# Optimization experiments

Hardware: AMD Instinct MI355X
Metric: run time of the kernel (lower is better)

## Reference

```python
import jax, jax.numpy as jnp
import numpy as np

EPS = 1e-5
GROUPS = 32


def conv2d(x, w, b):
    # x: [N,C,H,W], w: [O,I,3,3] (or 1x1), stride 1, padding 'same' for 3x3
    kh = w.shape[2]
    pad = (kh - 1) // 2
    y = jax.lax.conv_general_dilated(x, w, (1, 1), ((pad, pad), (pad, pad)),
                                     dimension_numbers=('NCHW', 'OIHW', 'NCHW'))
    return y + b[None, :, None, None]


def group_norm(x, g, b):
    N, C, H, W = x.shape
    xr = x.reshape(N, GROUPS, C // GROUPS, H, W)
    mu = xr.mean(axis=(2, 3, 4), keepdims=True)
    var = xr.var(axis=(2, 3, 4), keepdims=True)
    xr = (xr - mu) / jnp.sqrt(var + EPS)
    return xr.reshape(N, C, H, W) * g[None, :, None, None] + b[None, :, None, None]


def batch_norm(x, g, b):
    # training-mode BatchNorm2d: batch statistics over (N,H,W)
    mu = x.mean(axis=(0, 2, 3), keepdims=True)
    var = x.var(axis=(0, 2, 3), keepdims=True)
    return (x - mu) / jnp.sqrt(var + EPS) * g[None, :, None, None] + b[None, :, None, None]


def binary_activation(x):
    # STE: forward sign(x), backward through piecewise poly out3
    out_fwd = jnp.sign(x)
    m1 = (x < -1).astype(x.dtype)
    m2 = (x < 0).astype(x.dtype)
    m3 = (x < 1).astype(x.dtype)
    out1 = -1.0 * m1 + (x * x + 2.0 * x) * (1.0 - m1)
    out2 = out1 * m2 + (-x * x + 2.0 * x) * (1.0 - m2)
    out3 = out2 * m3 + 1.0 * (1.0 - m3)
    return jax.lax.stop_gradient(out_fwd - out3) + out3


def hard_binary_conv(x, w, b):
    # per-output-channel scaling * sign(w), STE through clipped weights
    scale = jax.lax.stop_gradient(jnp.mean(jnp.abs(w), axis=(1, 2, 3), keepdims=True))
    bw_ng = scale * jnp.sign(w)
    clipped = jnp.clip(w, -1.0, 1.0)
    bw = jax.lax.stop_gradient(bw_ng - clipped) + clipped
    return conv2d(x, bw, b)


def learnable_bias(x, emb, w, b):
    bias = jax.nn.silu(emb) @ w.T + b  # [B, C]
    return x + bias[:, :, None, None]


def _forward(c, x, emb,
             rb_gn1_g, rb_gn1_b, rb_conv1_w, rb_conv1_b, rb_emb_w, rb_emb_b,
             rb_gn2_g, rb_gn2_b, rb_conv2_w, rb_conv2_b,
             m1_w, m1_b, bconv_w, bconv_b, bn_g, bn_b,
             m2_w, m2_b, prelu_a, m3_w, m3_b):
    # ResBlock (skip = Identity since out_channels == channels)
    h = conv2d(jax.nn.silu(group_norm(c, rb_gn1_g, rb_gn1_b)), rb_conv1_w, rb_conv1_b)
    eo = jax.nn.silu(emb) @ rb_emb_w.T + rb_emb_b          # [B, 2*C]
    scale, shift = jnp.split(eo[:, :, None, None], 2, axis=1)
    h = group_norm(h, rb_gn2_g, rb_gn2_b) * (1.0 + scale) + shift
    h = conv2d(jax.nn.silu(h), rb_conv2_w, rb_conv2_b)
    c2 = c + h
    # concat + bias + STE binarize + binary conv + BN + channel-pool residual + PReLU
    xc = jnp.concatenate([x, c2], axis=1)                   # [B, 2C, H, W]
    out = learnable_bias(xc, emb, m1_w, m1_b)
    out = binary_activation(out)
    out = hard_binary_conv(out, bconv_w, bconv_b)
    out = batch_norm(out, bn_g, bn_b)
    N, C2, H, W = xc.shape
    out = out + xc.reshape(N, C2 // 2, 2, H, W).mean(axis=2)  # channel mean pooling
    out = learnable_bias(out, emb, m2_w, m2_b)
    out = jnp.where(out >= 0, out, prelu_a[None, :, None, None] * out)  # PReLU
    out = learnable_bias(out, emb, m3_w, m3_b)
    return out


def setup_inputs() -> dict:
    key = jax.random.key(0)
    ks = jax.random.split(key, 24)
    B, C, EMB, H, W = 8, 128, 512, 64, 64
    IN2 = 2 * C
    n = lambda k, s, sc=0.05: jax.random.normal(k, s, dtype=jnp.float32) * sc
    return {
        'c': jax.random.normal(ks[0], (B, C, H, W), dtype=jnp.float32),
        'x': jax.random.normal(ks[1], (B, C, H, W), dtype=jnp.float32),
        'emb': jax.random.normal(ks[2], (B, EMB), dtype=jnp.float32),
        'rb_gn1_g': jnp.ones((C,), jnp.float32), 'rb_gn1_b': jnp.zeros((C,), jnp.float32),
        'rb_conv1_w': n(ks[3], (C, C, 3, 3)), 'rb_conv1_b': n(ks[4], (C,)),
        'rb_emb_w': n(ks[5], (2 * C, EMB)), 'rb_emb_b': n(ks[6], (2 * C,)),
        'rb_gn2_g': jnp.ones((C,), jnp.float32), 'rb_gn2_b': jnp.zeros((C,), jnp.float32),
        'rb_conv2_w': n(ks[7], (C, C, 3, 3)), 'rb_conv2_b': n(ks[8], (C,)),
        'm1_w': n(ks[9], (IN2, EMB)), 'm1_b': n(ks[10], (IN2,)),
        'bconv_w': jax.random.uniform(ks[11], (C, IN2, 3, 3), dtype=jnp.float32) * 0.001,
        'bconv_b': n(ks[12], (C,)),
        'bn_g': jnp.ones((C,), jnp.float32), 'bn_b': jnp.zeros((C,), jnp.float32),
        'm2_w': n(ks[13], (C, EMB)), 'm2_b': n(ks[14], (C,)),
        'prelu_a': jnp.full((C,), 0.25, jnp.float32),
        'm3_w': n(ks[15], (C, EMB)), 'm3_b': n(ks[16], (C,)),
    }


def reference(c, x, emb,
              rb_gn1_g, rb_gn1_b, rb_conv1_w, rb_conv1_b, rb_emb_w, rb_emb_b,
              rb_gn2_g, rb_gn2_b, rb_conv2_w, rb_conv2_b,
              m1_w, m1_b, bconv_w, bconv_b, bn_g, bn_b,
              m2_w, m2_b, prelu_a, m3_w, m3_b):
    return _forward(c, x, emb,
                    rb_gn1_g, rb_gn1_b, rb_conv1_w, rb_conv1_b, rb_emb_w, rb_emb_b,
                    rb_gn2_g, rb_gn2_b, rb_conv2_w, rb_conv2_b,
                    m1_w, m1_b, bconv_w, bconv_b, bn_g, bn_b,
                    m2_w, m2_b, prelu_a, m3_w, m3_b)
```

## Files before the change

kernel.cpp:

```cpp
#include <hip/hip_runtime.h>
#include <stdint.h>


#define B_   8
#define C_   128
#define C2_  256
#define HW_  4096
#define EMB_ 512
#define EPS_ 1e-5f

typedef int   v16i __attribute__((ext_vector_type(16)));
typedef float v16f __attribute__((ext_vector_type(16)));
typedef short v8s  __attribute__((ext_vector_type(8)));
typedef int   v4i  __attribute__((ext_vector_type(4)));

#define COLB 272
#define LDSZ (3 * 66 * COLB)

__device__ __forceinline__ float silu(float v) {
    return v * __builtin_amdgcn_rcpf(1.f + __expf(-v));
}
__device__ __forceinline__ unsigned short f2bf(float f) {
    unsigned int x = __float_as_uint(f);
    return (unsigned short)((x + 0x7FFFu + ((x >> 16) & 1u)) >> 16);
}
__device__ __forceinline__ int8_t sgn8(float v) {
    return (v > 0.f) ? (int8_t)1 : ((v < 0.f) ? (int8_t)(-1) : (int8_t)0);
}

__global__ __launch_bounds__(256) void k_prep(
    const float* __restrict__ w, int8_t* __restrict__ sgn,
    float* __restrict__ alpha, float* __restrict__ bnS, float* __restrict__ bnQ,
    float* __restrict__ gnS, float* __restrict__ gnQ,
    const float* __restrict__ w1, const float* __restrict__ w2,
    unsigned short* __restrict__ Wc1, unsigned short* __restrict__ Wc2,
    const float* __restrict__ emb,
    const float* __restrict__ ew, const float* __restrict__ ebb,
    const float* __restrict__ m1w, const float* __restrict__ m1b,
    const float* __restrict__ m2w, const float* __restrict__ m2b,
    const float* __restrict__ m3w, const float* __restrict__ m3b,
    float* __restrict__ eo, float* __restrict__ b1,
    float* __restrict__ b2, float* __restrict__ b3,
    const float* __restrict__ gin, const float* __restrict__ g1w,
    const float* __restrict__ g1b, unsigned short* __restrict__ act1) {
    __shared__ float red[256];
    const int blk = blockIdx.x, tid = threadIdx.x;
    if (blk < 128) {
        const int o = blk;
        if (o == 0 && tid < 128) { bnS[tid] = 0.f; bnQ[tid] = 0.f; }
        if (o == 1) { gnS[tid] = 0.f; }
        if (o == 2) { gnQ[tid] = 0.f; }
        const float* wr = w + (size_t)o * (C2_ * 9);
        float s = 0.f;
        for (int i = tid; i < C2_ * 9; i += 256) s += fabsf(wr[i]);
        red[tid] = s;
        __syncthreads();
        for (int st = 128; st > 0; st >>= 1) {
            if (tid < st) red[tid] += red[tid + st];
            __syncthreads();
        }
        if (tid == 0) alpha[o] = red[0] / (float)(C2_ * 9);
        for (int kk = 0; kk < 9; ++kk) {
            float v = wr[tid * 9 + kk];
            sgn[((size_t)(kk * 16 + (tid >> 4)) * C_ + o) * 16 + (tid & 15)] = sgn8(v);
        }
    } else if (blk < 704) {
        int i = (blk - 128) * 256 + tid;
        int co = i / (C_ * 9);
        int rem = i - co * (C_ * 9);
        int ci = rem / 9, kk = rem - ci * 9;
        size_t d = ((size_t)(kk * 16 + (ci >> 3)) * C_ + co) * 8 + (ci & 7);
        Wc1[d] = f2bf(w1[i]);
        Wc2[d] = f2bf(w2[i]);
    } else if (blk < 896) {
        const int o = (blk - 704) * 4 + (tid >> 6);
        const int l = tid & 63;
        const float* wv;
        float bias;
        float* dst;
        int dstride;
        if (o < 256)      { wv = ew  + (size_t)o * EMB_;              bias = ebb[o];    dst = eo + o;  dstride = 256; }
        else if (o < 512) { int r = o - 256; wv = m1w + (size_t)r * EMB_; bias = m1b[r]; dst = b1 + r; dstride = 256; }
        else if (o < 640) { int r = o - 512; wv = m2w + (size_t)r * EMB_; bias = m2b[r]; dst = b2 + r; dstride = 128; }
        else              { int r = o - 640; wv = m3w + (size_t)r * EMB_; bias = m3b[r]; dst = b3 + r; dstride = 128; }
        const float4 wa = *(const float4*)(wv + 8 * l);
        const float4 wb = *(const float4*)(wv + 8 * l + 4);
#pragma unroll
        for (int b = 0; b < B_; ++b) {
            const float* s = emb + b * EMB_ + 8 * l;
            float4 sa = *(const float4*)(s);
            float4 sb = *(const float4*)(s + 4);
            float p = wa.x * silu(sa.x) + wa.y * silu(sa.y) + wa.z * silu(sa.z) + wa.w * silu(sa.w) +
                      wb.x * silu(sb.x) + wb.y * silu(sb.y) + wb.z * silu(sb.z) + wb.w * silu(sb.w);
#pragma unroll
            for (int off = 32; off > 0; off >>= 1) p += __shfl_down(p, off, 64);
            if (l == 0) dst[b * dstride] = bias + p;
        }
    } else {
        const int bb = blk - 896;
        const int n = bb >> 5, grp = bb & 31;
        const size_t base = ((size_t)(n * C_ + grp * 4)) << 12;
        float sum = 0.f, sq = 0.f;
        const float4* in4 = (const float4*)(gin + base);
        for (int i = tid; i < 4096; i += 256) {
            float4 v = in4[i];
            sum += v.x + v.y + v.z + v.w;
            sq += v.x * v.x + v.y * v.y + v.z * v.z + v.w * v.w;
        }
#pragma unroll
        for (int off = 32; off > 0; off >>= 1) {
            sum += __shfl_xor(sum, off, 64);
            sq  += __shfl_xor(sq, off, 64);
        }
        if ((tid & 63) == 0) { red[tid >> 6] = sum; red[8 + (tid >> 6)] = sq; }
        __syncthreads();
        sum = red[0] + red[1] + red[2] + red[3];
        sq  = red[8] + red[9] + red[10] + red[11];
        const float mu = sum * (1.f / 16384.f);
        const float rstd = rsqrtf(sq * (1.f / 16384.f) - mu * mu + EPS_);
        float gg[4], bb4[4];
#pragma unroll
        for (int j = 0; j < 4; ++j) { gg[j] = g1w[grp * 4 + j]; bb4[j] = g1b[grp * 4 + j]; }
        for (int hw = tid; hw < HW_; hw += 256) {
            union { unsigned short u[4]; uint2 v; } pk;
#pragma unroll
            for (int j = 0; j < 4; ++j) {
                float v = gin[base + ((size_t)j << 12) + hw];
                pk.u[j] = f2bf(silu((v - mu) * rstd * gg[j] + bb4[j]));
            }
            *(uint2*)(act1 + ((size_t)(n * HW_ + hw)) * C_ + grp * 4) = pk.v;
        }
    }
}

__device__ __forceinline__ void stage_rows(char* lds, const char* rs0,
                                           const char* rs1, const char* rs2) {
    const int tid = threadIdx.x;
    const char* rs[3] = {rs0, rs1, rs2};
    if (tid < 96) {
        int r = tid / 32, q = tid & 31;
        int c = (q >> 4) ? 65 : 0, o = q & 15;
        *(float4*)(lds + (r * 66 + c) * COLB + o * 16) = make_float4(0.f, 0.f, 0.f, 0.f);
    }
#pragma unroll
    for (int u = 0; u < 12; ++u) {
        int idx = u * 256 + tid;
        int r = idx >> 10, rem = idx & 1023;
        int x = rem >> 4, o = rem & 15;
        char* dst = lds + (r * 66 + x + 1) * COLB + o * 16;
        if (rs[r]) *(float4*)dst = *(const float4*)(rs[r] + x * 256 + o * 16);
        else       *(float4*)dst = make_float4(0.f, 0.f, 0.f, 0.f);
    }
}

__global__ __launch_bounds__(256) void k_conv1(const unsigned short* __restrict__ act,
                                               const unsigned short* __restrict__ Wc,
                                               const float* __restrict__ bias,
                                               float* __restrict__ out,
                                               float* __restrict__ gnS,
                                               float* __restrict__ gnQ) {
    __shared__ __align__(16) char lds[LDSZ];
    const int y = blockIdx.x;
    const int n = blockIdx.y;
    const char* base = (const char*)(act + ((size_t)n * 64) * 64 * C_);
    stage_rows(lds,
               (y > 0)  ? base + (size_t)(y - 1) * 16384 : nullptr,
               base + (size_t)y * 16384,
               (y < 63) ? base + (size_t)(y + 1) * 16384 : nullptr);
    __syncthreads();

    const int w = threadIdx.x >> 6;
    const int l = threadIdx.x & 63;
    const int lm = l & 31;
    const int lh = l >> 5;

    v16f acc0, acc1;
#pragma unroll
    for (int i = 0; i < 16; ++i) { acc0[i] = 0.f; acc1[i] = 0.f; }

#pragma unroll
    for (int kk = 0; kk < 9; ++kk) {
        const int r = kk / 3, dx = kk % 3 - 1;
        const char* col0 = lds + (r * 66 + lm + 1 + dx) * COLB + 16 * lh;
        const char* col1 = col0 + 32 * COLB;
        const unsigned short* wbase = Wc + (size_t)(kk * 16 + lh) * C_ * 8 + (32 * w + lm) * 8;
#pragma unroll
        for (int cb = 0; cb < 8; ++cb) {
            v8s a = *(const v8s*)(wbase + (size_t)(2 * cb) * C_ * 8);
            v8s b0 = *(const v8s*)(col0 + 32 * cb);
            v8s b1 = *(const v8s*)(col1 + 32 * cb);
            acc0 = __builtin_amdgcn_mfma_f32_32x32x16_bf16(a, b0, acc0, 0, 0, 0);
            acc1 = __builtin_amdgcn_mfma_f32_32x32x16_bf16(a, b1, acc1, 0, 0, 0);
        }
    }
    float pr[16], qr[16];
#pragma unroll
    for (int r = 0; r < 16; ++r) {
        const int row = (r & 3) + 8 * (r >> 2) + 4 * lh;
        const int co = 32 * w + row;
        const float bv = bias[co];
        const size_t o = (((size_t)n * C_ + co) << 12) + (y << 6);
        float v0 = acc0[r] + bv, v1 = acc1[r] + bv;
        out[o + lm] = v0;
        out[o + 32 + lm] = v1;
        pr[r] = v0 + v1;
        qr[r] = v0 * v0 + v1 * v1;
    }
    __syncthreads();
    float* ldsS = (float*)lds;
    float* ldsQ = (float*)lds + 128;
#pragma unroll
    for (int r = 0; r < 16; ++r) {
        float p = pr[r], q = qr[r];
#pragma unroll
        for (int m = 16; m > 0; m >>= 1) {
            p += __shfl_xor(p, m, 64);
            q += __shfl_xor(q, m, 64);
        }
        if (lm == 0) {
            const int row = (r & 3) + 8 * (r >> 2) + 4 * lh;
            const int co = 32 * w + row;
            ldsS[co] = p;
            ldsQ[co] = q;
        }
    }
    __syncthreads();
    if (threadIdx.x < 32) {
        const int g = threadIdx.x;
        float p = ldsS[4 * g] + ldsS[4 * g + 1] + ldsS[4 * g + 2] + ldsS[4 * g + 3];
        float q = ldsQ[4 * g] + ldsQ[4 * g + 1] + ldsQ[4 * g + 2] + ldsQ[4 * g + 3];
        atomicAdd(&gnS[n * 32 + g], p);
        atomicAdd(&gnQ[n * 32 + g], q);
    }
}

__global__ __launch_bounds__(256) void k_conv2(const float* __restrict__ yin,
                                               const unsigned short* __restrict__ Wc,
                                               const float* __restrict__ bias,
                                               const float* __restrict__ res,
                                               const float* __restrict__ xin,
                                               const float* __restrict__ b1v,
                                               const float* __restrict__ eo,
                                               const float* __restrict__ g2,
                                               const float* __restrict__ bt2,
                                               const float* __restrict__ gnS,
                                               const float* __restrict__ gnQ,
                                               float* __restrict__ poolC2,
                                               int8_t* __restrict__ S) {
    __shared__ __align__(16) char lds[LDSZ];
    __shared__ float ldsA[128], ldsB[128];
    const int y = blockIdx.x;
    const int n = blockIdx.y;
    const int tid = threadIdx.x;

    if (tid < 128) {
        const int ch = tid, grp = tid >> 2;
        const float mu = gnS[n * 32 + grp] * (1.f / 16384.f);
        const float var = gnQ[n * 32 + grp] * (1.f / 16384.f) - mu * mu;
        const float rstd = rsqrtf(var + EPS_);
        const float gg = g2[ch] * rstd;
        const float sc = 1.f + eo[n * 256 + ch];
        ldsA[ch] = gg * sc;
        ldsB[ch] = (bt2[ch] - mu * gg) * sc + eo[n * 256 + 128 + ch];
    }
    if (tid < 96) {
        int r = tid / 32, q = tid & 31;
        int cpad = (q >> 4) ? 65 : 0, o = q & 15;
        *(float4*)(lds + (r * 66 + cpad) * COLB + o * 16) = make_float4(0.f, 0.f, 0.f, 0.f);
    }
    __syncthreads();

    const float* yb = yin + ((size_t)n * C_) * HW_ + (y << 6);
#pragma unroll 4
    for (int u = 0; u < 24; ++u) {
        int unit = u * 256 + tid;
        int r = unit >> 11, rem = unit & 2047;
        int ch = rem >> 4, seg = rem & 15;
        int yy = y - 1 + r;
        char* dst = lds + (r * 66 + 1 + seg) * COLB + ch * 2;
        if (yy >= 0 && yy < 64) {
            const float A = ldsA[ch], Bv = ldsB[ch];
            const float* src = yb + (size_t)ch * HW_ + (r - 1) * 64 + seg;
#pragma unroll
            for (int j = 0; j < 4; ++j)
                *(unsigned short*)(dst + (16 * j) * COLB) = f2bf(silu(src[16 * j] * A + Bv));
        } else {
#pragma unroll
            for (int j = 0; j < 4; ++j)
                *(unsigned short*)(dst + (16 * j) * COLB) = 0;
        }
    }
    __syncthreads();

    const int w = tid >> 6;
    const int l = tid & 63;
    const int lm = l & 31;
    const int lh = l >> 5;

    v16f acc0, acc1;
#pragma unroll
    for (int i = 0; i < 16; ++i) { acc0[i] = 0.f; acc1[i] = 0.f; }

#pragma unroll
    for (int kk = 0; kk < 9; ++kk) {
        const int r = kk / 3, dx = kk % 3 - 1;
        const char* col0 = lds + (r * 66 + lm + 1 + dx) * COLB + 16 * lh;
        const char* col1 = col0 + 32 * COLB;
        const unsigned short* wbase = Wc + (size_t)(kk * 16 + lh) * C_ * 8 + (32 * w + lm) * 8;
#pragma unroll
        for (int cb = 0; cb < 8; ++cb) {
            v8s a = *(const v8s*)(wbase + (size_t)(2 * cb) * C_ * 8);
            v8s b0 = *(const v8s*)(col0 + 32 * cb);
            v8s b1 = *(const v8s*)(col1 + 32 * cb);
            acc0 = __builtin_amdgcn_mfma_f32_32x32x16_bf16(a, b0, acc0, 0, 0, 0);
            acc1 = __builtin_amdgcn_mfma_f32_32x32x16_bf16(a, b1, acc1, 0, 0, 0);
        }
    }
    float c2v0[16], c2v1[16];
#pragma unroll
    for (int r = 0; r < 16; ++r) {
        const int row = (r & 3) + 8 * (r >> 2) + 4 * lh;
        const int co = 32 * w + row;
        const float bv = bias[co];
        const size_t o = (((size_t)n * C_ + co) << 12) + (y << 6);
        c2v0[r] = acc0[r] + bv + res[o + lm];
        c2v1[r] = acc1[r] + bv + res[o + 32 + lm];
    }
#pragma unroll
    for (int q = 0; q < 4; ++q) {
        const int pc = 16 * w + 4 * q + 2 * lh;
        const size_t po = (((size_t)n * 64 + pc) << 12) + (y << 6);
        poolC2[po + lm]             = 0.5f * (c2v0[4 * q] + c2v0[4 * q + 1]);
        poolC2[po + 32 + lm]        = 0.5f * (c2v1[4 * q] + c2v1[4 * q + 1]);
        poolC2[po + 4096 + lm]      = 0.5f * (c2v0[4 * q + 2] + c2v0[4 * q + 3]);
        poolC2[po + 4096 + 32 + lm] = 0.5f * (c2v1[4 * q + 2] + c2v1[4 * q + 3]);
    }

    __syncthreads();
#pragma unroll
    for (int q = 0; q < 4; ++q) {
        const int co0 = 32 * w + 8 * q + 4 * lh;
        const float b0 = b1v[n * 256 + 128 + co0];
        const float b1b = b1v[n * 256 + 128 + co0 + 1];
        const float b2b = b1v[n * 256 + 128 + co0 + 2];
        const float b3b = b1v[n * 256 + 128 + co0 + 3];
        union { int8_t b[4]; int u; } p0, p1;
        p0.b[0] = sgn8(c2v0[4 * q] + b0);  p1.b[0] = sgn8(c2v1[4 * q] + b0);
        p0.b[1] = sgn8(c2v0[4 * q + 1] + b1b); p1.b[1] = sgn8(c2v1[4 * q + 1] + b1b);
        p0.b[2] = sgn8(c2v0[4 * q + 2] + b2b); p1.b[2] = sgn8(c2v1[4 * q + 2] + b2b);
        p0.b[3] = sgn8(c2v0[4 * q + 3] + b3b); p1.b[3] = sgn8(c2v1[4 * q + 3] + b3b);
        *(int*)(lds + lm * COLB + 128 + co0) = p0.u;
        *(int*)(lds + (32 + lm) * COLB + 128 + co0) = p1.u;
    }
#pragma unroll
    for (int u = 0; u < 8; ++u) {
        int idx = u * 256 + tid;
        int ch = idx >> 4, seg = idx & 15;
        float4 v = *(const float4*)(xin + (((size_t)(n * C_ + ch)) << 12) + (y << 6) + 4 * seg);
        const float bv = b1v[n * 256 + ch];
        lds[(4 * seg) * COLB + ch]     = sgn8(v.x + bv);
        lds[(4 * seg + 1) * COLB + ch] = sgn8(v.y + bv);
        lds[(4 * seg + 2) * COLB + ch] = sgn8(v.z + bv);
        lds[(4 * seg + 3) * COLB + ch] = sgn8(v.w + bv);
    }
    __syncthreads();
    int8_t* Srow = S + ((size_t)(n * HW_) + (y << 6)) * C2_;
#pragma unroll
    for (int u = 0; u < 4; ++u) {
        int idx = u * 256 + tid;
        int px = idx >> 4, c16 = idx & 15;
        *(int4*)(Srow + (size_t)px * C2_ + 16 * c16) = *(const int4*)(lds + px * COLB + 16 * c16);
    }
}

__global__ __launch_bounds__(256) void k_bconv(const int8_t* __restrict__ S,
                                               const int8_t* __restrict__ Wk,
                                               const float* __restrict__ alpha,
                                               const float* __restrict__ bias,
                                               float* __restrict__ out,
                                               float* __restrict__ bnS,
                                               float* __restrict__ bnQ) {
    __shared__ __align__(16) char lds[LDSZ];
    const int y = blockIdx.x;
    const int n = blockIdx.y;
    const char* base = (const char*)(S + ((size_t)n * 64) * 64 * C2_);
    stage_rows(lds,
               (y > 0)  ? base + (size_t)(y - 1) * 16384 : nullptr,
               base + (size_t)y * 16384,
               (y < 63) ? base + (size_t)(y + 1) * 16384 : nullptr);
    __syncthreads();

    const int w = threadIdx.x >> 6;
    const int l = threadIdx.x & 63;
    const int lm = l & 31;
    const int lh = l >> 5;

    v16i acc0, acc1;
#pragma unroll
    for (int i = 0; i < 16; ++i) { acc0[i] = 0; acc1[i] = 0; }

#pragma unroll
    for (int kk = 0; kk < 9; ++kk) {
        const int r = kk / 3, dx = kk % 3 - 1;
        const char* col0 = lds + (r * 66 + lm + 1 + dx) * COLB + 16 * lh;
        const char* col1 = col0 + 32 * COLB;
        const int8_t* wbase = Wk + (size_t)(kk * 16 + lh) * C_ * 16 + (32 * w + lm) * 16;
#pragma unroll
        for (int s = 0; s < 8; ++s) {
            v4i a = *(const v4i*)(wbase + (size_t)(2 * s) * C_ * 16);
            v4i b0 = *(const v4i*)(col0 + 32 * s);
            v4i b1 = *(const v4i*)(col1 + 32 * s);
            acc0 = __builtin_amdgcn_mfma_i32_32x32x32_i8(a, b0, acc0, 0, 0, 0);
            acc1 = __builtin_amdgcn_mfma_i32_32x32x32_i8(a, b1, acc1, 0, 0, 0);
        }
    }

    float pr[16], qr[16];
#pragma unroll
    for (int r = 0; r < 16; ++r) {
        const int row = (r & 3) + 8 * (r >> 2) + 4 * lh;
        const int co = 32 * w + row;
        const float av = alpha[co], bv = bias[co];
        const size_t o = (((size_t)n * C_ + co) << 12) + (y << 6);
        float v0 = av * (float)acc0[r] + bv;
        float v1 = av * (float)acc1[r] + bv;
        out[o + lm]      = v0;
        out[o + 32 + lm] = v1;
        pr[r] = v0 + v1;
        qr[r] = v0 * v0 + v1 * v1;
    }
    __syncthreads();
    float* ldsS = (float*)lds;
    float* ldsQ = (float*)lds + 128;
#pragma unroll
    for (int r = 0; r < 16; ++r) {
        float p = pr[r], q = qr[r];
#pragma unroll
        for (int m = 16; m > 0; m >>= 1) {
            p += __shfl_xor(p, m, 64);
            q += __shfl_xor(q, m, 64);
        }
        if (lm == 0) {
            const int row = (r & 3) + 8 * (r >> 2) + 4 * lh;
            const int co = 32 * w + row;
            ldsS[co] = p;
            ldsQ[co] = q;
        }
    }
    __syncthreads();
    if (threadIdx.x < 128) {
        atomicAdd(&bnS[threadIdx.x], ldsS[threadIdx.x]);
        atomicAdd(&bnQ[threadIdx.x], ldsQ[threadIdx.x]);
    }
}

__global__ __launch_bounds__(256) void k_final(const float* __restrict__ y3,
                                               const float* __restrict__ x,
                                               const float* __restrict__ poolC2,
                                               const float* __restrict__ bnS,
                                               const float* __restrict__ bnQ,
                                               const float* __restrict__ bng,
                                               const float* __restrict__ bnb,
                                               const float* __restrict__ b2v,
                                               const float* __restrict__ pa,
                                               const float* __restrict__ b3v,
                                               float* __restrict__ out) {
    const int idx4 = blockIdx.x * 256 + threadIdx.x;
    const int hw = (idx4 & 1023) * 4;
    const int cb = idx4 >> 10;
    const int co = cb & 127;
    const int n = cb >> 7;
    const float mu = bnS[co] * (1.f / 32768.f);
    const float var = bnQ[co] * (1.f / 32768.f) - mu * mu;
    const float rstd = rsqrtf(var + EPS_);
    const float gm = rstd * bng[co];
    const float bt = bnb[co] - mu * gm;
    const size_t obase = (((size_t)(n * C_ + co)) << 12) + hw;
    float4 v = *(const float4*)(y3 + obase);
    v.x = v.x * gm + bt; v.y = v.y * gm + bt; v.z = v.z * gm + bt; v.w = v.w * gm + bt;

    float4 pv;
    if (co < 64) {
        const int ch0 = 2 * co;
        float4 pA = *(const float4*)(x + (((size_t)(n * C_ + ch0)) << 12) + hw);
        float4 pB = *(const float4*)(x + (((size_t)(n * C_ + ch0 + 1)) << 12) + hw);
        pv.x = 0.5f * (pA.x + pB.x); pv.y = 0.5f * (pA.y + pB.y);
        pv.z = 0.5f * (pA.z + pB.z); pv.w = 0.5f * (pA.w + pB.w);
    } else {
        pv = *(const float4*)(poolC2 + (((size_t)(n * 64 + co - 64)) << 12) + hw);
    }
    const float bias2 = b2v[n * 128 + co];
    const float aP = pa[co];
    const float bias3 = b3v[n * 128 + co];
    float4 r;
    float t;
    t = v.x + pv.x + bias2; t = (t >= 0.f) ? t : aP * t; r.x = t + bias3;
    t = v.y + pv.y + bias2; t = (t >= 0.f) ? t : aP * t; r.y = t + bias3;
    t = v.z + pv.z + bias2; t = (t >= 0.f) ? t : aP * t; r.z = t + bias3;
    t = v.w + pv.w + bias2; t = (t >= 0.f) ? t : aP * t; r.w = t + bias3;
    *(float4*)(out + obase) = r;
}

extern "C" void kernel_launch(void* const* d_in, const int* in_sizes, int n_in,
                              void* d_out, int out_size, void* d_ws, size_t ws_size,
                              hipStream_t stream) {
    const float* c       = (const float*)d_in[0];
    const float* x       = (const float*)d_in[1];
    const float* emb     = (const float*)d_in[2];
    const float* gn1_g   = (const float*)d_in[3];
    const float* gn1_b   = (const float*)d_in[4];
    const float* conv1_w = (const float*)d_in[5];
    const float* conv1_b = (const float*)d_in[6];
    const float* emb_w   = (const float*)d_in[7];
    const float* emb_b   = (const float*)d_in[8];
    const float* gn2_g   = (const float*)d_in[9];
    const float* gn2_b   = (const float*)d_in[10];
    const float* conv2_w = (const float*)d_in[11];
    const float* conv2_b = (const float*)d_in[12];
    const float* m1_w    = (const float*)d_in[13];
    const float* m1_b    = (const float*)d_in[14];
    const float* bconv_w = (const float*)d_in[15];
    const float* bconv_b = (const float*)d_in[16];
    const float* bn_g    = (const float*)d_in[17];
    const float* bn_b    = (const float*)d_in[18];
    const float* m2_w    = (const float*)d_in[19];
    const float* m2_b    = (const float*)d_in[20];
    const float* prelu_a = (const float*)d_in[21];
    const float* m3_w    = (const float*)d_in[22];
    const float* m3_b    = (const float*)d_in[23];
    float* out = (float*)d_out;

    float* ws = (float*)d_ws;
    const size_t NCHW = (size_t)B_ * C_ * HW_;
    float*  poolC2 = ws;
    float*  y_buf = ws + NCHW;
    unsigned short* actA = (unsigned short*)(ws + 2 * NCHW);
    int8_t* S     = (int8_t*)(ws + 2 * NCHW);
    int8_t* sgn   = (int8_t*)(ws + 2 * NCHW + NCHW / 2);
    unsigned short* Wc1 = (unsigned short*)(ws + 2 * NCHW + NCHW / 2 + 73728);
    unsigned short* Wc2 = Wc1 + C_ * C_ * 9;
    float*  alpha = ws + 2 * NCHW + NCHW / 2 + 73728 + 2 * 73728;
    float*  eo    = alpha + 128;
    float*  b1v   = eo + B_ * 256;
    float*  b2v   = b1v + B_ * 256;
    float*  b3v   = b2v + B_ * 128;
    float*  bnS   = b3v + B_ * 128;
    float*  bnQ   = bnS + 128;
    float*  gnS   = bnQ + 128;
    float*  gnQ   = gnS + 256;

    k_prep<<<1152, 256, 0, stream>>>(bconv_w, sgn, alpha, bnS, bnQ, gnS, gnQ,
                                     conv1_w, conv2_w, Wc1, Wc2,
                                     emb, emb_w, emb_b, m1_w, m1_b, m2_w, m2_b,
                                     m3_w, m3_b, eo, b1v, b2v, b3v,
                                     c, gn1_g, gn1_b, actA);
    k_conv1<<<dim3(64, B_), 256, 0, stream>>>(actA, Wc1, conv1_b, y_buf, gnS, gnQ);
    k_conv2<<<dim3(64, B_), 256, 0, stream>>>(y_buf, Wc2, conv2_b, c, x, b1v, eo,
                                              gn2_g, gn2_b, gnS, gnQ, poolC2, S);
    k_bconv<<<dim3(64, B_), 256, 0, stream>>>(S, sgn, alpha, bconv_b, y_buf, bnS, bnQ);
    k_final<<<NCHW / 1024, 256, 0, stream>>>(y_buf, x, poolC2, bnS, bnQ, bn_g, bn_b,
                                             b2v, prelu_a, b3v, out);
}
```

Baseline: 237.4 us.

## Fuse all stages into one persistent kernel with software grid barriers

Replaces five separate kernel launches with a single 512-block persistent kernel. The stages are separated by a software global barrier built on atomic counters in workspace. The final BN/PReLU epilogue runs in registers after the last barrier, so the y_buf round-trip and the separate k_final pass are gone. This aims to cut launch gaps and one full-tensor memory pass. In exchange it depends on all 512 blocks being co-resident (launch_bounds 256,2) and adds spin-wait barrier cost.

```diff
diff --git a/kernel.cpp b/kernel.cpp
--- a/kernel.cpp
+++ b/kernel.cpp
@@ -8,6 +8,8 @@
 #define HW_  4096
 #define EMB_ 512
 #define EPS_ 1e-5f
+#define NBLK_ 512
+#define MAGIC_ 0x5CA1AB1EF00DFEEDULL
 
 typedef int   v16i __attribute__((ext_vector_type(16)));
 typedef float v16f __attribute__((ext_vector_type(16)));
@@ -28,80 +30,84 @@
     return (v > 0.f) ? (int8_t)1 : ((v < 0.f) ? (int8_t)(-1) : (int8_t)0);
 }
 
-__global__ __launch_bounds__(256) void k_prep(
-    const float* __restrict__ w, int8_t* __restrict__ sgn,
-    float* __restrict__ alpha, float* __restrict__ bnS, float* __restrict__ bnQ,
-    float* __restrict__ gnS, float* __restrict__ gnQ,
-    const float* __restrict__ w1, const float* __restrict__ w2,
-    unsigned short* __restrict__ Wc1, unsigned short* __restrict__ Wc2,
+__device__ __forceinline__ void gbarrier(unsigned long long* ready,
+                                         unsigned long long* cnt) {
+    __syncthreads();
+    if (threadIdx.x == 0) {
+        __threadfence();
+        while (__hip_atomic_load(ready, __ATOMIC_ACQUIRE,
+                                 __HIP_MEMORY_SCOPE_AGENT) != MAGIC_)
+            __builtin_amdgcn_s_sleep(2);
+        unsigned long long v = __hip_atomic_fetch_add(
+            cnt, 1ULL, __ATOMIC_ACQ_REL, __HIP_MEMORY_SCOPE_AGENT);
+        unsigned long long target = (v / NBLK_ + 1ULL) * (unsigned long long)NBLK_;
+        while (__hip_atomic_load(cnt, __ATOMIC_RELAXED,
+                                 __HIP_MEMORY_SCOPE_AGENT) < target)
+            __builtin_amdgcn_s_sleep(2);
+        __threadfence();
+    }
+    __syncthreads();
+}
+
+__global__ __launch_bounds__(256, 2) void k_fused(
+    const float* __restrict__ cin, const float* __restrict__ xin,
     const float* __restrict__ emb,
+    const float* __restrict__ g1w, const float* __restrict__ g1b,
+    const float* __restrict__ w1, const float* __restrict__ c1b,
     const float* __restrict__ ew, const float* __restrict__ ebb,
+    const float* __restrict__ g2w, const float* __restrict__ g2b,
+    const float* __restrict__ w2, const float* __restrict__ c2b,
     const float* __restrict__ m1w, const float* __restrict__ m1b,
+    const float* __restrict__ wq, const float* __restrict__ bqb,
+    const float* __restrict__ bng, const float* __restrict__ bnb,
     const float* __restrict__ m2w, const float* __restrict__ m2b,
+    const float* __restrict__ pa,
     const float* __restrict__ m3w, const float* __restrict__ m3b,
-    float* __restrict__ eo, float* __restrict__ b1,
-    float* __restrict__ b2, float* __restrict__ b3,
-    const float* __restrict__ gin, const float* __restrict__ g1w,
-    const float* __restrict__ g1b, unsigned short* __restrict__ act1) {
-    __shared__ float red[256];
-    const int blk = blockIdx.x, tid = threadIdx.x;
-    if (blk < 128) {
-        const int o = blk;
-        if (o == 0 && tid < 128) { bnS[tid] = 0.f; bnQ[tid] = 0.f; }
-        if (o == 1) { gnS[tid] = 0.f; }
-        if (o == 2) { gnQ[tid] = 0.f; }
-        const float* wr = w + (size_t)o * (C2_ * 9);
-        float s = 0.f;
-        for (int i = tid; i < C2_ * 9; i += 256) s += fabsf(wr[i]);
-        red[tid] = s;
-        __syncthreads();
-        for (int st = 128; st > 0; st >>= 1) {
-            if (tid < st) red[tid] += red[tid + st];
-            __syncthreads();
-        }
-        if (tid == 0) alpha[o] = red[0] / (float)(C2_ * 9);
-        for (int kk = 0; kk < 9; ++kk) {
-            float v = wr[tid * 9 + kk];
-            sgn[((size_t)(kk * 16 + (tid >> 4)) * C_ + o) * 16 + (tid & 15)] = sgn8(v);
-        }
-    } else if (blk < 704) {
-        int i = (blk - 128) * 256 + tid;
-        int co = i / (C_ * 9);
-        int rem = i - co * (C_ * 9);
-        int ci = rem / 9, kk = rem - ci * 9;
-        size_t d = ((size_t)(kk * 16 + (ci >> 3)) * C_ + co) * 8 + (ci & 7);
-        Wc1[d] = f2bf(w1[i]);
-        Wc2[d] = f2bf(w2[i]);
-    } else if (blk < 896) {
-        const int o = (blk - 704) * 4 + (tid >> 6);
-        const int l = tid & 63;
-        const float* wv;
-        float bias;
-        float* dst;
-        int dstride;
-        if (o < 256)      { wv = ew  + (size_t)o * EMB_;              bias = ebb[o];    dst = eo + o;  dstride = 256; }
-        else if (o < 512) { int r = o - 256; wv = m1w + (size_t)r * EMB_; bias = m1b[r]; dst = b1 + r; dstride = 256; }
-        else if (o < 640) { int r = o - 512; wv = m2w + (size_t)r * EMB_; bias = m2b[r]; dst = b2 + r; dstride = 128; }
-        else              { int r = o - 640; wv = m3w + (size_t)r * EMB_; bias = m3b[r]; dst = b3 + r; dstride = 128; }
-        const float4 wa = *(const float4*)(wv + 8 * l);
-        const float4 wb = *(const float4*)(wv + 8 * l + 4);
-#pragma unroll
-        for (int b = 0; b < B_; ++b) {
-            const float* s = emb + b * EMB_ + 8 * l;
-            float4 sa = *(const float4*)(s);
-            float4 sb = *(const float4*)(s + 4);
-            float p = wa.x * silu(sa.x) + wa.y * silu(sa.y) + wa.z * silu(sa.z) + wa.w * silu(sa.w) +
-                      wb.x * silu(sb.x) + wb.y * silu(sb.y) + wb.z * silu(sb.z) + wb.w * silu(sb.w);
-#pragma unroll
-            for (int off = 32; off > 0; off >>= 1) p += __shfl_down(p, off, 64);
-            if (l == 0) dst[b * dstride] = bias + p;
-        }
-    } else {
-        const int bb = blk - 896;
-        const int n = bb >> 5, grp = bb & 31;
+    float* __restrict__ out, float* __restrict__ ws) {
+    __shared__ __align__(16) char lds[LDSZ];
+    __shared__ float ldsA[128], ldsB[128];
+
+    const size_t NCHW = (size_t)B_ * C_ * HW_;
+    float* poolC2 = ws;
+    float* y_buf  = ws + NCHW;
+    unsigned short* actA = (unsigned short*)(ws + 2 * NCHW);
+    int8_t* S     = (int8_t*)(ws + 2 * NCHW);
+    int8_t* sgn   = (int8_t*)(ws + 2 * NCHW + NCHW / 2);
+    unsigned short* Wc1 = (unsigned short*)(ws + 2 * NCHW + NCHW / 2 + 73728);
+    unsigned short* Wc2 = Wc1 + C_ * C_ * 9;
+    float* alpha = ws + 2 * NCHW + NCHW / 2 + 73728 + 2 * 73728;
+    float* eo    = alpha + 128;
+    float* b1v   = eo + B_ * 256;
+    float* b2v   = b1v + B_ * 256;
+    float* b3v   = b2v + B_ * 128;
+    float* bnS   = b3v + B_ * 128;
+    float* bnQ   = bnS + 128;
+    float* gnS   = bnQ + 128;
+    float* gnQ   = gnS + 256;
+    unsigned long long* bar = (unsigned long long*)(gnQ + 256);
+    unsigned long long* ready = bar;
+    unsigned long long* cnt   = bar + 1;
+
+    const int blk = blockIdx.x;
+    const int tid = threadIdx.x;
+
+    if (blk == 0 && tid == 0) {
+        if (__hip_atomic_load(ready, __ATOMIC_RELAXED,
+                              __HIP_MEMORY_SCOPE_AGENT) != MAGIC_) {
+            for (int i = 0; i < 4; ++i)
+                __hip_atomic_store(&cnt[i], 0ULL, __ATOMIC_RELAXED,
+                                   __HIP_MEMORY_SCOPE_AGENT);
+            __hip_atomic_store(ready, MAGIC_, __ATOMIC_RELEASE,
+                               __HIP_MEMORY_SCOPE_AGENT);
+        }
+    }
+
+    if (blk < 256) {
+        float* red = (float*)lds;
+        const int n = blk >> 5, grp = blk & 31;
         const size_t base = ((size_t)(n * C_ + grp * 4)) << 12;
         float sum = 0.f, sq = 0.f;
-        const float4* in4 = (const float4*)(gin + base);
+        const float4* in4 = (const float4*)(cin + base);
         for (int i = tid; i < 4096; i += 256) {
             float4 v = in4[i];
             sum += v.x + v.y + v.z + v.w;
@@ -125,380 +131,415 @@
             union { unsigned short u[4]; uint2 v; } pk;
 #pragma unroll
             for (int j = 0; j < 4; ++j) {
-                float v = gin[base + ((size_t)j << 12) + hw];
+                float v = cin[base + ((size_t)j << 12) + hw];
                 pk.u[j] = f2bf(silu((v - mu) * rstd * gg[j] + bb4[j]));
             }
-            *(uint2*)(act1 + ((size_t)(n * HW_ + hw)) * C_ + grp * 4) = pk.v;
-        }
-    }
-}
-
-__device__ __forceinline__ void stage_rows(char* lds, const char* rs0,
-                                           const char* rs1, const char* rs2) {
-    const int tid = threadIdx.x;
-    const char* rs[3] = {rs0, rs1, rs2};
-    if (tid < 96) {
-        int r = tid / 32, q = tid & 31;
-        int c = (q >> 4) ? 65 : 0, o = q & 15;
-        *(float4*)(lds + (r * 66 + c) * COLB + o * 16) = make_float4(0.f, 0.f, 0.f, 0.f);
-    }
-#pragma unroll
-    for (int u = 0; u < 12; ++u) {
-        int idx = u * 256 + tid;
-        int r = idx >> 10, rem = idx & 1023;
-        int x = rem >> 4, o = rem & 15;
-        char* dst = lds + (r * 66 + x + 1) * COLB + o * 16;
-        if (rs[r]) *(float4*)dst = *(const float4*)(rs[r] + x * 256 + o * 16);
-        else       *(float4*)dst = make_float4(0.f, 0.f, 0.f, 0.f);
-    }
-}
-
-__global__ __launch_bounds__(256) void k_conv1(const unsigned short* __restrict__ act,
-                                               const unsigned short* __restrict__ Wc,
-                                               const float* __restrict__ bias,
-                                               float* __restrict__ out,
-                                               float* __restrict__ gnS,
-                                               float* __restrict__ gnQ) {
-    __shared__ __align__(16) char lds[LDSZ];
-    const int y = blockIdx.x;
-    const int n = blockIdx.y;
-    const char* base = (const char*)(act + ((size_t)n * 64) * 64 * C_);
-    stage_rows(lds,
-               (y > 0)  ? base + (size_t)(y - 1) * 16384 : nullptr,
-               base + (size_t)y * 16384,
-               (y < 63) ? base + (size_t)(y + 1) * 16384 : nullptr);
-    __syncthreads();
-
-    const int w = threadIdx.x >> 6;
-    const int l = threadIdx.x & 63;
-    const int lm = l & 31;
-    const int lh = l >> 5;
-
-    v16f acc0, acc1;
-#pragma unroll
-    for (int i = 0; i < 16; ++i) { acc0[i] = 0.f; acc1[i] = 0.f; }
-
-#pragma unroll
-    for (int kk = 0; kk < 9; ++kk) {
-        const int r = kk / 3, dx = kk % 3 - 1;
-        const char* col0 = lds + (r * 66 + lm + 1 + dx) * COLB + 16 * lh;
-        const char* col1 = col0 + 32 * COLB;
-        const unsigned short* wbase = Wc + (size_t)(kk * 16 + lh) * C_ * 8 + (32 * w + lm) * 8;
-#pragma unroll
-        for (int cb = 0; cb < 8; ++cb) {
-            v8s a = *(const v8s*)(wbase + (size_t)(2 * cb) * C_ * 8);
-            v8s b0 = *(const v8s*)(col0 + 32 * cb);
-            v8s b1 = *(const v8s*)(col1 + 32 * cb);
-            acc0 = __builtin_amdgcn_mfma_f32_32x32x16_bf16(a, b0, acc0, 0, 0, 0);
-            acc1 = __builtin_amdgcn_mfma_f32_32x32x16_bf16(a, b1, acc1, 0, 0, 0);
-        }
-    }
-    float pr[16], qr[16];
-#pragma unroll
-    for (int r = 0; r < 16; ++r) {
-        const int row = (r & 3) + 8 * (r >> 2) + 4 * lh;
-        const int co = 32 * w + row;
-        const float bv = bias[co];
-        const size_t o = (((size_t)n * C_ + co) << 12) + (y << 6);
-        float v0 = acc0[r] + bv, v1 = acc1[r] + bv;
-        out[o + lm] = v0;
-        out[o + 32 + lm] = v1;
-        pr[r] = v0 + v1;
-        qr[r] = v0 * v0 + v1 * v1;
-    }
-    __syncthreads();
-    float* ldsS = (float*)lds;
-    float* ldsQ = (float*)lds + 128;
-#pragma unroll
-    for (int r = 0; r < 16; ++r) {
-        float p = pr[r], q = qr[r];
-#pragma unroll
-        for (int m = 16; m > 0; m >>= 1) {
-            p += __shfl_xor(p, m, 64);
-            q += __shfl_xor(q, m, 64);
-        }
-        if (lm == 0) {
+            *(uint2*)(actA + ((size_t)(n * HW_ + hw)) * C_ + grp * 4) = pk.v;
+        }
+    } else if (blk < 384) {
+        float* red = (float*)lds;
+        const int o = blk - 256;
+        if (o == 0 && tid < 128) { bnS[tid] = 0.f; bnQ[tid] = 0.f; }
+        if (o == 1) gnS[tid] = 0.f;
+        if (o == 2) gnQ[tid] = 0.f;
+        const float* wr = wq + (size_t)o * (C2_ * 9);
+        float s = 0.f;
+        for (int i = tid; i < C2_ * 9; i += 256) s += fabsf(wr[i]);
+        red[tid] = s;
+        __syncthreads();
+        for (int st = 128; st > 0; st >>= 1) {
+            if (tid < st) red[tid] += red[tid + st];
+            __syncthreads();
+        }
+        if (tid == 0) alpha[o] = red[0] / (float)(C2_ * 9);
+        for (int kk = 0; kk < 9; ++kk) {
+            float v = wr[tid * 9 + kk];
+            sgn[((size_t)(kk * 16 + (tid >> 4)) * C_ + o) * 16 + (tid & 15)] = sgn8(v);
+        }
+    } else {
+        for (int i = (blk - 384) * 256 + tid; i < C_ * C_ * 9; i += 128 * 256) {
+            int co = i / (C_ * 9);
+            int rem = i - co * (C_ * 9);
+            int ci = rem / 9, kk = rem - ci * 9;
+            size_t d = ((size_t)(kk * 16 + (ci >> 3)) * C_ + co) * 8 + (ci & 7);
+            Wc1[d] = f2bf(w1[i]);
+            Wc2[d] = f2bf(w2[i]);
+        }
+    }
+    if (blk >= 256) {
+        const int o = (blk - 256) * 4 + (tid >> 6);
+        if (o < 768) {
+            const int l = tid & 63;
+            const float* wv;
+            float bias;
+            float* dst;
+            int dstride;
+            if (o < 256)      { wv = ew  + (size_t)o * EMB_;              bias = ebb[o];    dst = eo + o;   dstride = 256; }
+            else if (o < 512) { int r = o - 256; wv = m1w + (size_t)r * EMB_; bias = m1b[r]; dst = b1v + r; dstride = 256; }
+            else if (o < 640) { int r = o - 512; wv = m2w + (size_t)r * EMB_; bias = m2b[r]; dst = b2v + r; dstride = 128; }
+            else              { int r = o - 640; wv = m3w + (size_t)r * EMB_; bias = m3b[r]; dst = b3v + r; dstride = 128; }
+            const float4 wa = *(const float4*)(wv + 8 * l);
+            const float4 wb = *(const float4*)(wv + 8 * l + 4);
+#pragma unroll
+            for (int b = 0; b < B_; ++b) {
+                const float* sp = emb + b * EMB_ + 8 * l;
+                float4 sa = *(const float4*)(sp);
+                float4 sb = *(const float4*)(sp + 4);
+                float p = wa.x * silu(sa.x) + wa.y * silu(sa.y) + wa.z * silu(sa.z) + wa.w * silu(sa.w) +
+                          wb.x * silu(sb.x) + wb.y * silu(sb.y) + wb.z * silu(sb.z) + wb.w * silu(sb.w);
+#pragma unroll
+                for (int off = 32; off > 0; off >>= 1) p += __shfl_down(p, off, 64);
+                if (l == 0) dst[b * dstride] = bias + p;
+            }
+        }
+    }
+    gbarrier(ready, &cnt[0]);
+
+    {
+        const int y = blk & 63;
+        const int n = blk >> 6;
+        const char* base = (const char*)(actA + ((size_t)n * 64) * 64 * C_);
+        {
+            const char* rs[3] = {
+                (y > 0)  ? base + (size_t)(y - 1) * 16384 : nullptr,
+                base + (size_t)y * 16384,
+                (y < 63) ? base + (size_t)(y + 1) * 16384 : nullptr };
+            if (tid < 96) {
+                int r = tid / 32, q = tid & 31;
+                int c = (q >> 4) ? 65 : 0, o = q & 15;
+                *(float4*)(lds + (r * 66 + c) * COLB + o * 16) = make_float4(0.f, 0.f, 0.f, 0.f);
+            }
+#pragma unroll
+            for (int u = 0; u < 12; ++u) {
+                int idx = u * 256 + tid;
+                int r = idx >> 10, rem = idx & 1023;
+                int x = rem >> 4, o = rem & 15;
+                char* dst = lds + (r * 66 + x + 1) * COLB + o * 16;
+                if (rs[r]) *(float4*)dst = *(const float4*)(rs[r] + x * 256 + o * 16);
+                else       *(float4*)dst = make_float4(0.f, 0.f, 0.f, 0.f);
+            }
+        }
+        __syncthreads();
+
+        const int w = tid >> 6;
+        const int l = tid & 63;
+        const int lm = l & 31;
+        const int lh = l >> 5;
+
+        v16f acc0, acc1;
+#pragma unroll
+        for (int i = 0; i < 16; ++i) { acc0[i] = 0.f; acc1[i] = 0.f; }
+
+#pragma unroll
+        for (int kk = 0; kk < 9; ++kk) {
+            const int r = kk / 3, dx = kk % 3 - 1;
+            const char* col0 = lds + (r * 66 + lm + 1 + dx) * COLB + 16 * lh;
+            const char* col1 = col0 + 32 * COLB;
+            const unsigned short* wbase = Wc1 + (size_t)(kk * 16 + lh) * C_ * 8 + (32 * w + lm) * 8;
+#pragma unroll
+            for (int cb = 0; cb < 8; ++cb) {
+                v8s a = *(const v8s*)(wbase + (size_t)(2 * cb) * C_ * 8);
+                v8s b0 = *(const v8s*)(col0 + 32 * cb);
+                v8s b1 = *(const v8s*)(col1 + 32 * cb);
+                acc0 = __builtin_amdgcn_mfma_f32_32x32x16_bf16(a, b0, acc0, 0, 0, 0);
+                acc1 = __builtin_amdgcn_mfma_f32_32x32x16_bf16(a, b1, acc1, 0, 0, 0);
+            }
+        }
+        float pr[16], qr[16];
+#pragma unroll
+        for (int r = 0; r < 16; ++r) {
             const int row = (r & 3) + 8 * (r >> 2) + 4 * lh;
             const int co = 32 * w + row;
-            ldsS[co] = p;
-            ldsQ[co] = q;
-        }
-    }
-    __syncthreads();
-    if (threadIdx.x < 32) {
-        const int g = threadIdx.x;
-        float p = ldsS[4 * g] + ldsS[4 * g + 1] + ldsS[4 * g + 2] + ldsS[4 * g + 3];
-        float q = ldsQ[4 * g] + ldsQ[4 * g + 1] + ldsQ[4 * g + 2] + ldsQ[4 * g + 3];
-        atomicAdd(&gnS[n * 32 + g], p);
-        atomicAdd(&gnQ[n * 32 + g], q);
-    }
-}
-
-__global__ __launch_bounds__(256) void k_conv2(const float* __restrict__ yin,
-                                               const unsigned short* __restrict__ Wc,
-                                               const float* __restrict__ bias,
-                                               const float* __restrict__ res,
-                                               const float* __restrict__ xin,
-                                               const float* __restrict__ b1v,
-                                               const float* __restrict__ eo,
-                                               const float* __restrict__ g2,
-                                               const float* __restrict__ bt2,
-                                               const float* __restrict__ gnS,
-                                               const float* __restrict__ gnQ,
-                                               float* __restrict__ poolC2,
-                                               int8_t* __restrict__ S) {
-    __shared__ __align__(16) char lds[LDSZ];
-    __shared__ float ldsA[128], ldsB[128];
-    const int y = blockIdx.x;
-    const int n = blockIdx.y;
-    const int tid = threadIdx.x;
-
-    if (tid < 128) {
-        const int ch = tid, grp = tid >> 2;
-        const float mu = gnS[n * 32 + grp] * (1.f / 16384.f);
-        const float var = gnQ[n * 32 + grp] * (1.f / 16384.f) - mu * mu;
-        const float rstd = rsqrtf(var + EPS_);
-        const float gg = g2[ch] * rstd;
-        const float sc = 1.f + eo[n * 256 + ch];
-        ldsA[ch] = gg * sc;
-        ldsB[ch] = (bt2[ch] - mu * gg) * sc + eo[n * 256 + 128 + ch];
-    }
-    if (tid < 96) {
-        int r = tid / 32, q = tid & 31;
-        int cpad = (q >> 4) ? 65 : 0, o = q & 15;
-        *(float4*)(lds + (r * 66 + cpad) * COLB + o * 16) = make_float4(0.f, 0.f, 0.f, 0.f);
-    }
-    __syncthreads();
-
-    const float* yb = yin + ((size_t)n * C_) * HW_ + (y << 6);
+            const float bv = c1b[co];
+            const size_t o = (((size_t)n * C_ + co) << 12) + (y << 6);
+            float v0 = acc0[r] + bv, v1 = acc1[r] + bv;
+            y_buf[o + lm] = v0;
+            y_buf[o + 32 + lm] = v1;
+            pr[r] = v0 + v1;
+            qr[r] = v0 * v0 + v1 * v1;
+        }
+        __syncthreads();
+        float* ldsS = (float*)lds;
+        float* ldsQ = (float*)lds + 128;
+#pragma unroll
+        for (int r = 0; r < 16; ++r) {
+            float p = pr[r], q = qr[r];
+#pragma unroll
+            for (int m = 16; m > 0; m >>= 1) {
+                p += __shfl_xor(p, m, 64);
+                q += __shfl_xor(q, m, 64);
+            }
+            if (lm == 0) {
+                const int row = (r & 3) + 8 * (r >> 2) + 4 * lh;
+                const int co = 32 * w + row;
+                ldsS[co] = p;
+                ldsQ[co] = q;
+            }
+        }
+        __syncthreads();
+        if (tid < 32) {
+            const int g = tid;
+            float p = ldsS[4 * g] + ldsS[4 * g + 1] + ldsS[4 * g + 2] + ldsS[4 * g + 3];
+            float q = ldsQ[4 * g] + ldsQ[4 * g + 1] + ldsQ[4 * g + 2] + ldsQ[4 * g + 3];
+            atomicAdd(&gnS[n * 32 + g], p);
+            atomicAdd(&gnQ[n * 32 + g], q);
+        }
+    }
+    gbarrier(ready, &cnt[1]);
+
+    {
+        const int y = blk & 63;
+        const int n = blk >> 6;
+
+        if (tid < 128) {
+            const int ch = tid, grp = tid >> 2;
+            const float mu = gnS[n * 32 + grp] * (1.f / 16384.f);
+            const float var = gnQ[n * 32 + grp] * (1.f / 16384.f) - mu * mu;
+            const float rstd = rsqrtf(var + EPS_);
+            const float gg = g2w[ch] * rstd;
+            const float sc = 1.f + eo[n * 256 + ch];
+            ldsA[ch] = gg * sc;
+            ldsB[ch] = (g2b[ch] - mu * gg) * sc + eo[n * 256 + 128 + ch];
+        }
+        if (tid < 96) {
+            int r = tid / 32, q = tid & 31;
+            int cpad = (q >> 4) ? 65 : 0, o = q & 15;
+            *(float4*)(lds + (r * 66 + cpad) * COLB + o * 16) = make_float4(0.f, 0.f, 0.f, 0.f);
+        }
+        __syncthreads();
+
+        const float* yb = y_buf + ((size_t)n * C_) * HW_ + (y << 6);
 #pragma unroll 4
-    for (int u = 0; u < 24; ++u) {
-        int unit = u * 256 + tid;
-        int r = unit >> 11, rem = unit & 2047;
-        int ch = rem >> 4, seg = rem & 15;
-        int yy = y - 1 + r;
-        char* dst = lds + (r * 66 + 1 + seg) * COLB + ch * 2;
-        if (yy >= 0 && yy < 64) {
-            const float A = ldsA[ch], Bv = ldsB[ch];
-            const float* src = yb + (size_t)ch * HW_ + (r - 1) * 64 + seg;
-#pragma unroll
-            for (int j = 0; j < 4; ++j)
-                *(unsigned short*)(dst + (16 * j) * COLB) = f2bf(silu(src[16 * j] * A + Bv));
-        } else {
-#pragma unroll
-            for (int j = 0; j < 4; ++j)
-                *(unsigned short*)(dst + (16 * j) * COLB) = 0;
-        }
-    }
-    __syncthreads();
-
-    const int w = tid >> 6;
-    const int l = tid & 63;
-    const int lm = l & 31;
-    const int lh = l >> 5;
-
-    v16f acc0, acc1;
-#pragma unroll
-    for (int i = 0; i < 16; ++i) { acc0[i] = 0.f; acc1[i] = 0.f; }
-
-#pragma unroll
-    for (int kk = 0; kk < 9; ++kk) {
-        const int r = kk / 3, dx = kk % 3 - 1;
-        const char* col0 = lds + (r * 66 + lm + 1 + dx) * COLB + 16 * lh;
-        const char* col1 = col0 + 32 * COLB;
-        const unsigned short* wbase = Wc + (size_t)(kk * 16 + lh) * C_ * 8 + (32 * w + lm) * 8;
-#pragma unroll
-        for (int cb = 0; cb < 8; ++cb) {
-            v8s a = *(const v8s*)(wbase + (size_t)(2 * cb) * C_ * 8);
-            v8s b0 = *(const v8s*)(col0 + 32 * cb);
-            v8s b1 = *(const v8s*)(col1 + 32 * cb);
-            acc0 = __builtin_amdgcn_mfma_f32_32x32x16_bf16(a, b0, acc0, 0, 0, 0);
-            acc1 = __builtin_amdgcn_mfma_f32_32x32x16_bf16(a, b1, acc1, 0, 0, 0);
-        }
-    }
-    float c2v0[16], c2v1[16];
-#pragma unroll
-    for (int r = 0; r < 16; ++r) {
-        const int row = (r & 3) + 8 * (r >> 2) + 4 * lh;
-        const int co = 32 * w + row;
-        const float bv = bias[co];
-        const size_t o = (((size_t)n * C_ + co) << 12) + (y << 6);
-        c2v0[r] = acc0[r] + bv + res[o + lm];
-        c2v1[r] = acc1[r] + bv + res[o + 32 + lm];
-    }
-#pragma unroll
-    for (int q = 0; q < 4; ++q) {
-        const int pc = 16 * w + 4 * q + 2 * lh;
-        const size_t po = (((size_t)n * 64 + pc) << 12) + (y << 6);
-        poolC2[po + lm]             = 0.5f * (c2v0[4 * q] + c2v0[4 * q + 1]);
-        poolC2[po + 32 + lm]        = 0.5f * (c2v1[4 * q] + c2v1[4 * q + 1]);
-        poolC2[po + 4096 + lm]      = 0.5f * (c2v0[4 * q + 2] + c2v0[4 * q + 3]);
-        poolC2[po + 4096 + 32 + lm] = 0.5f * (c2v1[4 * q + 2] + c2v1[4 * q + 3]);
-    }
-
-    __syncthreads();
-#pragma unroll
-    for (int q = 0; q < 4; ++q) {
-        const int co0 = 32 * w + 8 * q + 4 * lh;
-        const float b0 = b1v[n * 256 + 128 + co0];
-        const float b1b = b1v[n * 256 + 128 + co0 + 1];
-        const float b2b = b1v[n * 256 + 128 + co0 + 2];
-        const float b3b = b1v[n * 256 + 128 + co0 + 3];
-        union { int8_t b[4]; int u; } p0, p1;
-        p0.b[0] = sgn8(c2v0[4 * q] + b0);  p1.b[0] = sgn8(c2v1[4 * q] + b0);
-        p0.b[1] = sgn8(c2v0[4 * q + 1] + b1b); p1.b[1] = sgn8(c2v1[4 * q + 1] + b1b);
-        p0.b[2] = sgn8(c2v0[4 * q + 2] + b2b); p1.b[2] = sgn8(c2v1[4 * q + 2] + b2b);
-        p0.b[3] = sgn8(c2v0[4 * q + 3] + b3b); p1.b[3] = sgn8(c2v1[4 * q + 3] + b3b);
-        *(int*)(lds + lm * COLB + 128 + co0) = p0.u;
-        *(int*)(lds + (32 + lm) * COLB + 128 + co0) = p1.u;
-    }
-#pragma unroll
-    for (int u = 0; u < 8; ++u) {
-        int idx = u * 256 + tid;
-        int ch = idx >> 4, seg = idx & 15;
-        float4 v = *(const float4*)(xin + (((size_t)(n * C_ + ch)) << 12) + (y << 6) + 4 * seg);
-        const float bv = b1v[n * 256 + ch];
-        lds[(4 * seg) * COLB + ch]     = sgn8(v.x + bv);
-        lds[(4 * seg + 1) * COLB + ch] = sgn8(v.y + bv);
-        lds[(4 * seg + 2) * COLB + ch] = sgn8(v.z + bv);
-        lds[(4 * seg + 3) * COLB + ch] = sgn8(v.w + bv);
-    }
-    __syncthreads();
-    int8_t* Srow = S + ((size_t)(n * HW_) + (y << 6)) * C2_;
-#pragma unroll
-    for (int u = 0; u < 4; ++u) {
-        int idx = u * 256 + tid;
-        int px = idx >> 4, c16 = idx & 15;
-        *(int4*)(Srow + (size_t)px * C2_ + 16 * c16) = *(const int4*)(lds + px * COLB + 16 * c16);
-    }
-}
-
-__global__ __launch_bounds__(256) void k_bconv(const int8_t* __restrict__ S,
-                                               const int8_t* __restrict__ Wk,
-                                               const float* __restrict__ alpha,
-                                               const float* __restrict__ bias,
-                                               float* __restrict__ out,
-                                               float* __restrict__ bnS,
-                                               float* __restrict__ bnQ) {
-    __shared__ __align__(16) char lds[LDSZ];
-    const int y = blockIdx.x;
-    const int n = blockIdx.y;
-    const char* base = (const char*)(S + ((size_t)n * 64) * 64 * C2_);
-    stage_rows(lds,
-               (y > 0)  ? base + (size_t)(y - 1) * 16384 : nullptr,
-               base + (size_t)y * 16384,
-               (y < 63) ? base + (size_t)(y + 1) * 16384 : nullptr);
-    __syncthreads();
-
-    const int w = threadIdx.x >> 6;
-    const int l = threadIdx.x & 63;
-    const int lm = l & 31;
-    const int lh = l >> 5;
-
-    v16i acc0, acc1;
-#pragma unroll
-    for (int i = 0; i < 16; ++i) { acc0[i] = 0; acc1[i] = 0; }
-
-#pragma unroll
-    for (int kk = 0; kk < 9; ++kk) {
-        const int r = kk / 3, dx = kk % 3 - 1;
-        const char* col0 = lds + (r * 66 + lm + 1 + dx) * COLB + 16 * lh;
-        const char* col1 = col0 + 32 * COLB;
-        const int8_t* wbase = Wk + (size_t)(kk * 16 + lh) * C_ * 16 + (32 * w + lm) * 16;
-#pragma unroll
-        for (int s = 0; s < 8; ++s) {
-            v4i a = *(const v4i*)(wbase + (size_t)(2 * s) * C_ * 16);
-            v4i b0 = *(const v4i*)(col0 + 32 * s);
-            v4i b1 = *(const v4i*)(col1 + 32 * s);
-            acc0 = __builtin_amdgcn_mfma_i32_32x32x32_i8(a, b0, acc0, 0, 0, 0);
-            acc1 = __builtin_amdgcn_mfma_i32_32x32x32_i8(a, b1, acc1, 0, 0, 0);
-        }
-    }
-
-    float pr[16], qr[16];
-#pragma unroll
-    for (int r = 0; r < 16; ++r) {
-        const int row = (r & 3) + 8 * (r >> 2) + 4 * lh;
-        const int co = 32 * w + row;
-        const float av = alpha[co], bv = bias[co];
-        const size_t o = (((size_t)n * C_ + co) << 12) + (y << 6);
-        float v0 = av * (float)acc0[r] + bv;
-        float v1 = av * (float)acc1[r] + bv;
-        out[o + lm]      = v0;
-        out[o + 32 + lm] = v1;
-        pr[r] = v0 + v1;
-        qr[r] = v0 * v0 + v1 * v1;
-    }
-    __syncthreads();
-    float* ldsS = (float*)lds;
-    float* ldsQ = (float*)lds + 128;
-#pragma unroll
-    for (int r = 0; r < 16; ++r) {
-        float p = pr[r], q = qr[r];
-#pragma unroll
-        for (int m = 16; m > 0; m >>= 1) {
-            p += __shfl_xor(p, m, 64);
-            q += __shfl_xor(q, m, 64);
-        }
-        if (lm == 0) {
+        for (int u = 0; u < 24; ++u) {
+            int unit = u * 256 + tid;
+            int r = unit >> 11, rem = unit & 2047;
+            int ch = rem >> 4, seg = rem & 15;
+            int yy = y - 1 + r;
+            char* dst = lds + (r * 66 + 1 + seg) * COLB + ch * 2;
+            if (yy >= 0 && yy < 64) {
+                const float A = ldsA[ch], Bv = ldsB[ch];
+                const float* src = yb + (size_t)ch * HW_ + (r - 1) * 64 + seg;
+#pragma unroll
+                for (int j = 0; j < 4; ++j)
+                    *(unsigned short*)(dst + (16 * j) * COLB) = f2bf(silu(src[16 * j] * A + Bv));
+            } else {
+#pragma unroll
+                for (int j = 0; j < 4; ++j)
+                    *(unsigned short*)(dst + (16 * j) * COLB) = 0;
+            }
+        }
+        __syncthreads();
+
+        const int w = tid >> 6;
+        const int l = tid & 63;
+        const int lm = l & 31;
+        const int lh = l >> 5;
+
+        v16f acc0, acc1;
+#pragma unroll
+        for (int i = 0; i < 16; ++i) { acc0[i] = 0.f; acc1[i] = 0.f; }
+
+#pragma unroll
+        for (int kk = 0; kk < 9; ++kk) {
+            const int r = kk / 3, dx = kk % 3 - 1;
+            const char* col0 = lds + (r * 66 + lm + 1 + dx) * COLB + 16 * lh;
+            const char* col1 = col0 + 32 * COLB;
+            const unsigned short* wbase = Wc2 + (size_t)(kk * 16 + lh) * C_ * 8 + (32 * w + lm) * 8;
+#pragma unroll
+            for (int cb = 0; cb < 8; ++cb) {
+                v8s a = *(const v8s*)(wbase + (size_t)(2 * cb) * C_ * 8);
+                v8s b0 = *(const v8s*)(col0 + 32 * cb);
+                v8s b1 = *(const v8s*)(col1 + 32 * cb);
+                acc0 = __builtin_amdgcn_mfma_f32_32x32x16_bf16(a, b0, acc0, 0, 0, 0);
+                acc1 = __builtin_amdgcn_mfma_f32_32x32x16_bf16(a, b1, acc1, 0, 0, 0);
+            }
+        }
+        float c2v0[16], c2v1[16];
+#pragma unroll
+        for (int r = 0; r < 16; ++r) {
             const int row = (r & 3) + 8 * (r >> 2) + 4 * lh;
             const int co = 32 * w + row;
-            ldsS[co] = p;
-            ldsQ[co] = q;
-        }
-    }
-    __syncthreads();
-    if (threadIdx.x < 128) {
-        atomicAdd(&bnS[threadIdx.x], ldsS[threadIdx.x]);
-        atomicAdd(&bnQ[threadIdx.x], ldsQ[threadIdx.x]);
-    }
-}
-
-__global__ __launch_bounds__(256) void k_final(const float* __restrict__ y3,
-                                               const float* __restrict__ x,
-                                               const float* __restrict__ poolC2,
-                                               const float* __restrict__ bnS,
-                                               const float* __restrict__ bnQ,
-                                               const float* __restrict__ bng,
-                                               const float* __restrict__ bnb,
-                                               const float* __restrict__ b2v,
-                                               const float* __restrict__ pa,
-                                               const float* __restrict__ b3v,
-                                               float* __restrict__ out) {
-    const int idx4 = blockIdx.x * 256 + threadIdx.x;
-    const int hw = (idx4 & 1023) * 4;
-    const int cb = idx4 >> 10;
-    const int co = cb & 127;
-    const int n = cb >> 7;
-    const float mu = bnS[co] * (1.f / 32768.f);
-    const float var = bnQ[co] * (1.f / 32768.f) - mu * mu;
-    const float rstd = rsqrtf(var + EPS_);
-    const float gm = rstd * bng[co];
-    const float bt = bnb[co] - mu * gm;
-    const size_t obase = (((size_t)(n * C_ + co)) << 12) + hw;
-    float4 v = *(const float4*)(y3 + obase);
-    v.x = v.x * gm + bt; v.y = v.y * gm + bt; v.z = v.z * gm + bt; v.w = v.w * gm + bt;
-
-    float4 pv;
-    if (co < 64) {
-        const int ch0 = 2 * co;
-        float4 pA = *(const float4*)(x + (((size_t)(n * C_ + ch0)) << 12) + hw);
-        float4 pB = *(const float4*)(x + (((size_t)(n * C_ + ch0 + 1)) << 12) + hw);
-        pv.x = 0.5f * (pA.x + pB.x); pv.y = 0.5f * (pA.y + pB.y);
-        pv.z = 0.5f * (pA.z + pB.z); pv.w = 0.5f * (pA.w + pB.w);
-    } else {
-        pv = *(const float4*)(poolC2 + (((size_t)(n * 64 + co - 64)) << 12) + hw);
-    }
-    const float bias2 = b2v[n * 128 + co];
-    const float aP = pa[co];
-    const float bias3 = b3v[n * 128 + co];
-    float4 r;
-    float t;
-    t = v.x + pv.x + bias2; t = (t >= 0.f) ? t : aP * t; r.x = t + bias3;
-    t = v.y + pv.y + bias2; t = (t >= 0.f) ? t : aP * t; r.y = t + bias3;
-    t = v.z + pv.z + bias2; t = (t >= 0.f) ? t : aP * t; r.z = t + bias3;
-    t = v.w + pv.w + bias2; t = (t >= 0.f) ? t : aP * t; r.w = t + bias3;
-    *(float4*)(out + obase) = r;
+            const float bv = c2b[co];
+            const size_t o = (((size_t)n * C_ + co) << 12) + (y << 6);
+            c2v0[r] = acc0[r] + bv + cin[o + lm];
+            c2v1[r] = acc1[r] + bv + cin[o + 32 + lm];
+        }
+#pragma unroll
+        for (int q = 0; q < 4; ++q) {
+            const int pc = 16 * w + 4 * q + 2 * lh;
+            const size_t po = (((size_t)n * 64 + pc) << 12) + (y << 6);
+            poolC2[po + lm]             = 0.5f * (c2v0[4 * q] + c2v0[4 * q + 1]);
+            poolC2[po + 32 + lm]        = 0.5f * (c2v1[4 * q] + c2v1[4 * q + 1]);
+            poolC2[po + 4096 + lm]      = 0.5f * (c2v0[4 * q + 2] + c2v0[4 * q + 3]);
+            poolC2[po + 4096 + 32 + lm] = 0.5f * (c2v1[4 * q + 2] + c2v1[4 * q + 3]);
+        }
+
+        __syncthreads();
+#pragma unroll
+        for (int q = 0; q < 4; ++q) {
+            const int co0 = 32 * w + 8 * q + 4 * lh;
+            const float b0 = b1v[n * 256 + 128 + co0];
+            const float b1b = b1v[n * 256 + 128 + co0 + 1];
+            const float b2b = b1v[n * 256 + 128 + co0 + 2];
+            const float b3b = b1v[n * 256 + 128 + co0 + 3];
+            union { int8_t b[4]; int u; } p0, p1;
+            p0.b[0] = sgn8(c2v0[4 * q] + b0);      p1.b[0] = sgn8(c2v1[4 * q] + b0);
+            p0.b[1] = sgn8(c2v0[4 * q + 1] + b1b); p1.b[1] = sgn8(c2v1[4 * q + 1] + b1b);
+            p0.b[2] = sgn8(c2v0[4 * q + 2] + b2b); p1.b[2] = sgn8(c2v1[4 * q + 2] + b2b);
+            p0.b[3] = sgn8(c2v0[4 * q + 3] + b3b); p1.b[3] = sgn8(c2v1[4 * q + 3] + b3b);
+            *(int*)(lds + lm * COLB + 128 + co0) = p0.u;
+            *(int*)(lds + (32 + lm) * COLB + 128 + co0) = p1.u;
+        }
+#pragma unroll
+        for (int u = 0; u < 8; ++u) {
+            int idx = u * 256 + tid;
+            int ch = idx >> 4, seg = idx & 15;
+            float4 v = *(const float4*)(xin + (((size_t)(n * C_ + ch)) << 12) + (y << 6) + 4 * seg);
+            const float bv = b1v[n * 256 + ch];
+            lds[(4 * seg) * COLB + ch]     = sgn8(v.x + bv);
+            lds[(4 * seg + 1) * COLB + ch] = sgn8(v.y + bv);
+            lds[(4 * seg + 2) * COLB + ch] = sgn8(v.z + bv);
+            lds[(4 * seg + 3) * COLB + ch] = sgn8(v.w + bv);
+        }
+        __syncthreads();
+        int8_t* Srow = S + ((size_t)(n * HW_) + (y << 6)) * C2_;
+#pragma unroll
+        for (int u = 0; u < 4; ++u) {
+            int idx = u * 256 + tid;
+            int px = idx >> 4, c16 = idx & 15;
+            *(int4*)(Srow + (size_t)px * C2_ + 16 * c16) = *(const int4*)(lds + px * COLB + 16 * c16);
+        }
+    }
+    gbarrier(ready, &cnt[2]);
+
+    {
+        const int y = blk & 63;
+        const int n = blk >> 6;
+        const char* base = (const char*)(S + ((size_t)n * 64) * 64 * C2_);
+        {
+            const char* rs[3] = {
+                (y > 0)  ? base + (size_t)(y - 1) * 16384 : nullptr,
+                base + (size_t)y * 16384,
+                (y < 63) ? base + (size_t)(y + 1) * 16384 : nullptr };
+            if (tid < 96) {
+                int r = tid / 32, q = tid & 31;
+                int c = (q >> 4) ? 65 : 0, o = q & 15;
+                *(float4*)(lds + (r * 66 + c) * COLB + o * 16) = make_float4(0.f, 0.f, 0.f, 0.f);
+            }
+#pragma unroll
+            for (int u = 0; u < 12; ++u) {
+                int idx = u * 256 + tid;
+                int r = idx >> 10, rem = idx & 1023;
+                int x = rem >> 4, o = rem & 15;
+                char* dst = lds + (r * 66 + x + 1) * COLB + o * 16;
+                if (rs[r]) *(float4*)dst = *(const float4*)(rs[r] + x * 256 + o * 16);
+                else       *(float4*)dst = make_float4(0.f, 0.f, 0.f, 0.f);
+            }
+        }
+        __syncthreads();
+
+        const int w = tid >> 6;
+        const int l = tid & 63;
+        const int lm = l & 31;
+        const int lh = l >> 5;
+
+        v16i acc0, acc1;
+#pragma unroll
+        for (int i = 0; i < 16; ++i) { acc0[i] = 0; acc1[i] = 0; }
+
+#pragma unroll
+        for (int kk = 0; kk < 9; ++kk) {
+            const int r = kk / 3, dx = kk % 3 - 1;
+            const char* col0 = lds + (r * 66 + lm + 1 + dx) * COLB + 16 * lh;
+            const char* col1 = col0 + 32 * COLB;
+            const int8_t* wbase = sgn + (size_t)(kk * 16 + lh) * C_ * 16 + (32 * w + lm) * 16;
+#pragma unroll
+            for (int s = 0; s < 8; ++s) {
+                v4i a = *(const v4i*)(wbase + (size_t)(2 * s) * C_ * 16);
+                v4i b0 = *(const v4i*)(col0 + 32 * s);
+                v4i b1 = *(const v4i*)(col1 + 32 * s);
+                acc0 = __builtin_amdgcn_mfma_i32_32x32x32_i8(a, b0, acc0, 0, 0, 0);
+                acc1 = __builtin_amdgcn_mfma_i32_32x32x32_i8(a, b1, acc1, 0, 0, 0);
+            }
+        }
+
+        float bv0[16], bv1[16], pr[16], qr[16];
+#pragma unroll
+        for (int r = 0; r < 16; ++r) {
+            const int row = (r & 3) + 8 * (r >> 2) + 4 * lh;
+            const int co = 32 * w + row;
+            const float av = alpha[co], bv = bqb[co];
+            float v0 = av * (float)acc0[r] + bv;
+            float v1 = av * (float)acc1[r] + bv;
+            bv0[r] = v0;
+            bv1[r] = v1;
+            pr[r] = v0 + v1;
+            qr[r] = v0 * v0 + v1 * v1;
+        }
+        __syncthreads();
+        float* ldsS = (float*)lds;
+        float* ldsQ = (float*)lds + 128;
+#pragma unroll
+        for (int r = 0; r < 16; ++r) {
+            float p = pr[r], q = qr[r];
+#pragma unroll
+            for (int m = 16; m > 0; m >>= 1) {
+                p += __shfl_xor(p, m, 64);
+                q += __shfl_xor(q, m, 64);
+            }
+            if (lm == 0) {
+                const int row = (r & 3) + 8 * (r >> 2) + 4 * lh;
+                const int co = 32 * w + row;
+                ldsS[co] = p;
+                ldsQ[co] = q;
+            }
+        }
+        __syncthreads();
+        if (tid < 128) {
+            atomicAdd(&bnS[tid], ldsS[tid]);
+            atomicAdd(&bnQ[tid], ldsQ[tid]);
+        }
+        gbarrier(ready, &cnt[3]);
+
+        float* ldsG  = (float*)lds;
+        float* ldsBt = (float*)lds + 128;
+        if (tid < 128) {
+            const int co = tid;
+            const float mu = bnS[co] * (1.f / 32768.f);
+            const float var = bnQ[co] * (1.f / 32768.f) - mu * mu;
+            const float rstd = rsqrtf(var + EPS_);
+            const float gm = rstd * bng[co];
+            ldsG[co]  = gm;
+            ldsBt[co] = bnb[co] - mu * gm;
+        }
+        __syncthreads();
+#pragma unroll
+        for (int r = 0; r < 16; ++r) {
+            const int row = (r & 3) + 8 * (r >> 2) + 4 * lh;
+            const int co = 32 * w + row;
+            const float gm = ldsG[co], bt = ldsBt[co];
+            float t0 = bv0[r] * gm + bt;
+            float t1 = bv1[r] * gm + bt;
+            float p0, p1;
+            if (co < 64) {
+                const size_t xb = (((size_t)(n * C_ + 2 * co)) << 12) + (y << 6);
+                p0 = 0.5f * (xin[xb + lm] + xin[xb + 4096 + lm]);
+                p1 = 0.5f * (xin[xb + 32 + lm] + xin[xb + 4096 + 32 + lm]);
+            } else {
+                const size_t pb = (((size_t)(n * 64 + co - 64)) << 12) + (y << 6);
+                p0 = poolC2[pb + lm];
+                p1 = poolC2[pb + 32 + lm];
+            }
+            const float bias2 = b2v[n * 128 + co];
+            const float aP = pa[co];
+            const float bias3 = b3v[n * 128 + co];
+            float o0 = t0 + p0 + bias2; o0 = (o0 >= 0.f) ? o0 : aP * o0; o0 += bias3;
+            float o1 = t1 + p1 + bias2; o1 = (o1 >= 0.f) ? o1 : aP * o1; o1 += bias3;
+            const size_t o = (((size_t)n * C_ + co) << 12) + (y << 6);
+            out[o + lm]      = o0;
+            out[o + 32 + lm] = o1;
+        }
+    }
 }
 
 extern "C" void kernel_launch(void* const* d_in, const int* in_sizes, int n_in,
@@ -529,35 +570,10 @@
     const float* m3_w    = (const float*)d_in[22];
     const float* m3_b    = (const float*)d_in[23];
     float* out = (float*)d_out;
-
-    float* ws = (float*)d_ws;
-    const size_t NCHW = (size_t)B_ * C_ * HW_;
-    float*  poolC2 = ws;
-    float*  y_buf = ws + NCHW;
-    unsigned short* actA = (unsigned short*)(ws + 2 * NCHW);
-    int8_t* S     = (int8_t*)(ws + 2 * NCHW);
-    int8_t* sgn   = (int8_t*)(ws + 2 * NCHW + NCHW / 2);
-    unsigned short* Wc1 = (unsigned short*)(ws + 2 * NCHW + NCHW / 2 + 73728);
-    unsigned short* Wc2 = Wc1 + C_ * C_ * 9;
-    float*  alpha = ws + 2 * NCHW + NCHW / 2 + 73728 + 2 * 73728;
-    float*  eo    = alpha + 128;
-    float*  b1v   = eo + B_ * 256;
-    float*  b2v   = b1v + B_ * 256;
-    float*  b3v   = b2v + B_ * 128;
-    float*  bnS   = b3v + B_ * 128;
-    float*  bnQ   = bnS + 128;
-    float*  gnS   = bnQ + 128;
-    float*  gnQ   = gnS + 256;
-
-    k_prep<<<1152, 256, 0, stream>>>(bconv_w, sgn, alpha, bnS, bnQ, gnS, gnQ,
-                                     conv1_w, conv2_w, Wc1, Wc2,
-                                     emb, emb_w, emb_b, m1_w, m1_b, m2_w, m2_b,
-                                     m3_w, m3_b, eo, b1v, b2v, b3v,
-                                     c, gn1_g, gn1_b, actA);
-    k_conv1<<<dim3(64, B_), 256, 0, stream>>>(actA, Wc1, conv1_b, y_buf, gnS, gnQ);
-    k_conv2<<<dim3(64, B_), 256, 0, stream>>>(y_buf, Wc2, conv2_b, c, x, b1v, eo,
-                                              gn2_g, gn2_b, gnS, gnQ, poolC2, S);
-    k_bconv<<<dim3(64, B_), 256, 0, stream>>>(S, sgn, alpha, bconv_b, y_buf, bnS, bnQ);
-    k_final<<<NCHW / 1024, 256, 0, stream>>>(y_buf, x, poolC2, bnS, bnQ, bn_g, bn_b,
-                                             b2v, prelu_a, b3v, out);
+    float* ws  = (float*)d_ws;
+
+    k_fused<<<NBLK_, 256, 0, stream>>>(
+        c, x, emb, gn1_g, gn1_b, conv1_w, conv1_b, emb_w, emb_b,
+        gn2_g, gn2_b, conv2_w, conv2_b, m1_w, m1_b, bconv_w, bconv_b,
+        bn_g, bn_b, m2_w, m2_b, prelu_a, m3_w, m3_b, out, ws);
 }
```

Result: slower. 470.4 us (+98.1%).
